# Kernel optimization log

Hardware: AMD Instinct MI355X
Metric: run time of the kernel (lower is better)

Reference implementation:

```python
import jax, jax.numpy as jnp
import numpy as np

B, T, D, H, NB, K, CDIM, CTX = 8, 4096, 3, 128, 6, 20, 128, 7


def setup_inputs() -> dict:
    key = jax.random.key(0)
    ks = jax.random.split(key, 16)
    s = 0.05
    inp = {
        'p': jax.random.normal(ks[0], (B, T, D), jnp.float32),
        'W_pos': jax.random.normal(ks[1], (D, H), jnp.float32) * s,
        'b_pos': jnp.zeros((H,), jnp.float32),
        # ResnetBlockFC(2H -> H): fc_0(2H,H), fc_1(H,H), shortcut(2H,H, no bias)
        'blk_W0': jax.random.normal(ks[2], (NB, 2 * H, H), jnp.float32) * s,
        'blk_b0': jnp.zeros((NB, H), jnp.float32),
        'blk_W1': jax.random.normal(ks[3], (NB, H, H), jnp.float32) * s,
        'blk_b1': jnp.zeros((NB, H), jnp.float32),
        'blk_Ws': jax.random.normal(ks[4], (NB, 2 * H, H), jnp.float32) * s,
        # Attention: score MLP on context (dim 7 -> 1), output proj (H -> H)
        'att_Wc': jax.random.normal(ks[5], (NB, CTX, 1), jnp.float32) * s,
        'att_bc': jnp.zeros((NB, 1), jnp.float32),
        'att_Wo': jax.random.normal(ks[6], (NB, H, H), jnp.float32) * s,
        'att_bo': jnp.zeros((NB, H), jnp.float32),
        'W_c': jax.random.normal(ks[7], (H, CDIM), jnp.float32) * s,
        'b_c': jnp.zeros((CDIM,), jnp.float32),
    }
    return inp


def _knn(p):
    # squared pairwise distances [B,T,T], top-K smallest
    sq = jnp.sum(p * p, axis=-1)  # [B,T]
    d2 = sq[:, :, None] + sq[:, None, :] - 2.0 * jnp.einsum('btd,bsd->bts', p, p)
    neg, idx = jax.lax.top_k(-d2, K)            # idx: [B,T,K]
    dis = jnp.sqrt(jnp.maximum(-neg, 1e-12))    # euclidean distance [B,T,K]
    return dis, idx


def _gather(c, idx):
    # c: [B,T,h], idx: [B,T,K] -> [B,T,K,h]  (vectorized pool_local)
    return jax.vmap(lambda ci, ii: ci[ii])(c, idx)


def _resnet_block(x, W0, b0, W1, b1, Ws):
    # occupancy-networks ResnetBlockFC: shortcut(x) + fc_1(relu(fc_0(relu(x))))
    h = jnp.maximum(x, 0.0) @ W0 + b0
    dx = jnp.maximum(h, 0.0) @ W1 + b1
    return x @ Ws + dx


def reference(p, W_pos, b_pos, blk_W0, blk_b0, blk_W1, blk_b1, blk_Ws,
              att_Wc, att_bc, att_Wo, att_bo, W_c, b_c):
    dis, idx = _knn(p)
    pooled_points = _gather(p, idx)                                   # [B,T,K,3]
    p_rep = jnp.broadcast_to(p[:, :, None, :], (B, T, K, D))
    context = jnp.concatenate([dis[..., None], pooled_points, p_rep], axis=-1)  # [B,T,K,7]

    net = p @ W_pos + b_pos                                           # [B,T,H]
    last_net = jnp.zeros_like(net)
    for i in range(NB):
        pooled = _gather(net, idx)                                    # [B,T,K,H]
        # attention over the K neighbors, weights from context
        scores = context @ att_Wc[i] + att_bc[i]                      # [B,T,K,1]
        w = jax.nn.softmax(scores, axis=2)
        att = jnp.sum(w * pooled, axis=2) @ att_Wo[i] + att_bo[i]     # [B,T,H]
        x = jnp.concatenate([net, att], axis=2)                       # [B,T,2H]
        net = _resnet_block(x, blk_W0[i], blk_b0[i], blk_W1[i], blk_b1[i], blk_Ws[i])
        net = net + last_net
        last_net = net
    return net @ W_c + b_c                                            # [B,T,c_dim]
```

## Files before the change

kernel.cpp:

```cpp
#include <hip/hip_runtime.h>
#include <hip/hip_bf16.h>
#include <math.h>

#define BB 8
#define TT 4096
#define HHD 128
#define NBK 6
#define KNN 20
#define BT (BB*TT)

typedef __attribute__((ext_vector_type(8))) short bf16x8;
typedef __attribute__((ext_vector_type(4))) float f32x4;

__device__ __forceinline__ float b2f(unsigned short u){
  return __uint_as_float(((unsigned int)u) << 16);
}
__device__ __forceinline__ unsigned short f2b(float f){
  unsigned int x = __float_as_uint(f);
  unsigned int r = (x + 0x7fffu + ((x >> 16) & 1u)) >> 16;
  return (unsigned short)r;
}
__device__ __forceinline__ float ldp(const void* base, int i, int f32m){
  return f32m ? ((const float*)base)[i] : b2f(((const unsigned short*)base)[i]);
}
__device__ __forceinline__ float lo2f(unsigned int u){ return __uint_as_float(u << 16); }
__device__ __forceinline__ float hi2f(unsigned int u){ return __uint_as_float(u & 0xffff0000u); }
__device__ __forceinline__ unsigned int relu2(unsigned int u){
  unsigned int s = u & 0x80008000u;
  unsigned int m = s | (s - (s >> 15));
  return u & ~m;
}
__device__ __forceinline__ bf16x8 relu8(bf16x8 x){
  union { bf16x8 v; unsigned int u[4]; } t; t.v = x;
  t.u[0] = relu2(t.u[0]); t.u[1] = relu2(t.u[1]);
  t.u[2] = relu2(t.u[2]); t.u[3] = relu2(t.u[3]);
  return t.v;
}

__global__ void k_detect(const unsigned short* __restrict__ wpos_raw, int* __restrict__ flag){
  if (threadIdx.x == 0 && blockIdx.x == 0) {
    int cnt = 0;
    for (int i = 0; i < 384; ++i) {
      unsigned int e = (wpos_raw[i] >> 7) & 0xFFu;
      if (e >= 0x90u) cnt++;
    }
    *flag = (cnt > 10) ? 1 : 0;
  }
}

__global__ __launch_bounds__(256) void k_prep_points(const void* __restrict__ p,
                                                     const int* __restrict__ flagp,
                                                     float4* __restrict__ pf4){
  int r = blockIdx.x*256 + threadIdx.x;
  if (r >= BT) return;
  int f32m = *flagp;
  float x = ldp(p, r*3+0, f32m), y = ldp(p, r*3+1, f32m), z = ldp(p, r*3+2, f32m);
  float sq = __fadd_rn(__fadd_rn(__fmul_rn(x,x), __fmul_rn(y,y)), __fmul_rn(z,z));
  pf4[r] = make_float4(x, y, z, sq);
}

__global__ __launch_bounds__(256) void k_net0(const float4* __restrict__ pf4,
                                              const void* __restrict__ Wpos,
                                              const void* __restrict__ bpos,
                                              const int* __restrict__ flagp,
                                              unsigned short* __restrict__ netA){
  int t = blockIdx.x*256 + threadIdx.x;
  int f32m = *flagp;
  int c = t & 127, r = t >> 7;
  float4 q = pf4[r];
  float v = ldp(bpos, c, f32m);
  v = fmaf(q.x, ldp(Wpos, c,       f32m), v);
  v = fmaf(q.y, ldp(Wpos, 128 + c, f32m), v);
  v = fmaf(q.z, ldp(Wpos, 256 + c, f32m), v);
  netA[t] = f2b(v);
}

__global__ __launch_bounds__(256) void k_transpose(const void* __restrict__ W0,
                                                   const void* __restrict__ W1,
                                                   const void* __restrict__ Ws,
                                                   const void* __restrict__ Wo,
                                                   const void* __restrict__ Wc,
                                                   const int* __restrict__ flagp,
                                                   unsigned short* __restrict__ wT){
  int t = blockIdx.x*256 + threadIdx.x;
  int f32m = *flagp;
  if (t < 196608) {
    int i = t >> 15; int rem = t & 32767; int n = rem >> 8; int k = rem & 255;
    wT[t] = f2b(ldp(W0, i*32768 + k*128 + n, f32m));
  } else if (t < 294912) {
    int u = t - 196608; int i = u >> 14; int rem = u & 16383; int n = rem >> 7; int k = rem & 127;
    wT[t] = f2b(ldp(W1, i*16384 + k*128 + n, f32m));
  } else if (t < 491520) {
    int u = t - 294912; int i = u >> 15; int rem = u & 32767; int n = rem >> 8; int k = rem & 255;
    wT[t] = f2b(ldp(Ws, i*32768 + k*128 + n, f32m));
  } else if (t < 589824) {
    int u = t - 491520; int i = u >> 14; int rem = u & 16383; int n = rem >> 7; int k = rem & 127;
    wT[t] = f2b(ldp(Wo, i*16384 + k*128 + n, f32m));
  } else if (t < 606208) {
    int u = t - 589824; int n = u >> 7; int k = u & 127;
    wT[t] = f2b(ldp(Wc, k*128 + n, f32m));
  }
}

#define INS(act, dv, iv) do { bool A_ = (act); float D_ = (dv); int I_ = (iv);        \
  _Pragma("unroll")                                                                    \
  for (int j = 19; j >= 1; --j) {                                                      \
    bool cj = A_ && (D_ < ld[j]); bool cm = A_ && (D_ < ld[j-1]);                      \
    ld[j] = cj ? (cm ? ld[j-1] : D_) : ld[j];                                          \
    li[j] = cj ? (cm ? li[j-1] : I_) : li[j];                                          \
  }                                                                                    \
  { bool c0 = A_ && (D_ < ld[0]); ld[0] = c0 ? D_ : ld[0]; li[0] = c0 ? I_ : li[0]; } \
} while(0)

__global__ __launch_bounds__(256) void k_knn(const float4* __restrict__ pf4,
                                             const void* __restrict__ Wc,
                                             const void* __restrict__ bc,
                                             const int* __restrict__ flagp,
                                             unsigned short* __restrict__ idx16,
                                             unsigned short* __restrict__ wsoftb){
  __shared__ char smem[40960];
  float4* tile = (float4*)smem;
  float*  lsd  = (float*)smem;
  int*    lsi  = (int*)(smem + 20480);

  int tid  = threadIdx.x;
  int part = tid >> 6, lane = tid & 63;
  int rq   = blockIdx.x*64 + lane;
  int b    = rq >> 12;
  int f32m = *flagp;
  float4 q = pf4[rq];

  float ld[20]; int li[20];
  #pragma unroll
  for (int j = 0; j < 20; ++j) { ld[j] = 3.0e38f; li[j] = 0; }
  float thresh = 3.0e38f;
  float bd0=0.f,bd1=0.f,bd2=0.f,bd3=0.f; int bi0=0,bi1=0,bi2=0,bi3=0; int cnt=0;

  for (int ch = 0; ch < 4; ++ch) {
    __syncthreads();
    {
      const float4* src = pf4 + (b << 12) + part*1024 + ch*256;
      tile[part*256 + lane      ] = src[lane      ];
      tile[part*256 + lane +  64] = src[lane +  64];
      tile[part*256 + lane + 128] = src[lane + 128];
      tile[part*256 + lane + 192] = src[lane + 192];
    }
    __syncthreads();
    int baseI = part*1024 + ch*256;
    for (int j = 0; j < 256; ++j) {
      float4 pt = tile[part*256 + j];
      float dot = __fadd_rn(__fadd_rn(__fmul_rn(q.x,pt.x), __fmul_rn(q.y,pt.y)),
                            __fmul_rn(q.z,pt.z));
      float d2  = __fsub_rn(__fadd_rn(q.w, pt.w), __fmul_rn(2.0f, dot));
      bool take = d2 < thresh;
      int  gi   = baseI + j;
      bool t0 = take && (cnt == 0); bd0 = t0 ? d2 : bd0; bi0 = t0 ? gi : bi0;
      bool t1 = take && (cnt == 1); bd1 = t1 ? d2 : bd1; bi1 = t1 ? gi : bi1;
      bool t2 = take && (cnt == 2); bd2 = t2 ? d2 : bd2; bi2 = t2 ? gi : bi2;
      bool t3 = take && (cnt == 3); bd3 = t3 ? d2 : bd3; bi3 = t3 ? gi : bi3;
      cnt += take ? 1 : 0;
      if (__ballot(cnt >= 4)) {
        INS(cnt > 0, bd0, bi0); INS(cnt > 1, bd1, bi1);
        INS(cnt > 2, bd2, bi2); INS(cnt > 3, bd3, bi3);
        cnt = 0; thresh = ld[19];
      }
    }
  }
  INS(cnt > 0, bd0, bi0); INS(cnt > 1, bd1, bi1);
  INS(cnt > 2, bd2, bi2); INS(cnt > 3, bd3, bi3);

  __syncthreads();
  #pragma unroll
  for (int j = 0; j < 20; ++j) { lsd[tid*20 + j] = ld[j]; lsi[tid*20 + j] = li[j]; }
  __syncthreads();

  if (tid < 64) {
    int p0 = tid*20, p1 = (64+tid)*20, p2 = (128+tid)*20, p3 = (192+tid)*20;
    int i0=0, i1=0, i2=0, i3=0;
    float dis[20]; int outi[20];
    #pragma unroll 4
    for (int o = 0; o < 20; ++o) {
      float d0 = lsd[p0+i0], d1 = lsd[p1+i1], d2v = lsd[p2+i2], d3 = lsd[p3+i3];
      float bd = d0; int sel = 0;
      if (d1  < bd) { bd = d1;  sel = 1; }
      if (d2v < bd) { bd = d2v; sel = 2; }
      if (d3  < bd) { bd = d3;  sel = 3; }
      int bi = (sel==0) ? lsi[p0+i0] : (sel==1) ? lsi[p1+i1] : (sel==2) ? lsi[p2+i2] : lsi[p3+i3];
      i0 += (sel==0); i1 += (sel==1); i2 += (sel==2); i3 += (sel==3);
      dis[o] = sqrtf(fmaxf(bd, 1e-12f));
      outi[o] = bi;
    }
    float nx[20], ny[20], nz[20];
    #pragma unroll 4
    for (int k = 0; k < 20; ++k) {
      idx16[rq*20 + k] = (unsigned short)outi[k];
      float4 pp = pf4[(b << 12) + outi[k]];
      nx[k] = pp.x; ny[k] = pp.y; nz[k] = pp.z;
    }
    for (int i = 0; i < NBK; ++i) {
      float w0 = ldp(Wc,i*7+0,f32m), w1 = ldp(Wc,i*7+1,f32m), w2 = ldp(Wc,i*7+2,f32m);
      float w3 = ldp(Wc,i*7+3,f32m), w4 = ldp(Wc,i*7+4,f32m), w5 = ldp(Wc,i*7+5,f32m);
      float w6 = ldp(Wc,i*7+6,f32m);
      float bci = ldp(bc,i,f32m);
      float s[20]; float mx = -3.0e38f;
      #pragma unroll
      for (int k = 0; k < 20; ++k) {
        float v = bci;
        v = fmaf(dis[k], w0, v);
        v = fmaf(nx[k], w1, v); v = fmaf(ny[k], w2, v); v = fmaf(nz[k], w3, v);
        v = fmaf(q.x, w4, v);  v = fmaf(q.y, w5, v);  v = fmaf(q.z, w6, v);
        s[k] = v; mx = fmaxf(mx, v);
      }
      float sum = 0.f;
      #pragma unroll
      for (int k = 0; k < 20; ++k) { float e = __expf(s[k] - mx); s[k] = e; sum += e; }
      float inv = 1.0f / sum;
      #pragma unroll
      for (int k = 0; k < 20; ++k) wsoftb[(rq*6 + i)*20 + k] = f2b(s[k]*inv);
    }
  }
}

__global__ __launch_bounds__(256) void k_block(const unsigned short* __restrict__ netIn,
                                               unsigned short* __restrict__ netOut,
                                               const unsigned short* __restrict__ idx16,
                                               const unsigned short* __restrict__ wsoftb,
                                               const unsigned short* __restrict__ wT,
                                               const void* __restrict__ b0s,
                                               const void* __restrict__ b1s,
                                               const void* __restrict__ bos,
                                               const int* __restrict__ flagp,
                                               int iblk, int hasResid){
  __shared__ unsigned short ldsA[2][16*136];
  __shared__ unsigned short ldsH[2][16*136];
  int tid = threadIdx.x;
  int f32m = *flagp;
  int w = tid >> 6, lane = tid & 63;
  int t = w >> 1;
  int c = w & 1;
  int b  = blockIdx.x & 7;
  int r0 = (b << 12) + ((blockIdx.x >> 3) << 5) + (t << 4);
  const unsigned short* W0T = wT + iblk*32768;
  const unsigned short* W1T = wT + 196608 + iblk*16384;
  const unsigned short* WsT = wT + 294912 + iblk*32768;
  const unsigned short* WoT = wT + 491520 + iblk*16384;
  int m = lane & 15, qd = lane >> 4;

  {
    int r = lane >> 2, cg = lane & 3;
    int grow = r0 + r;
    int cbase = c*64 + cg*16;
    float acc[16];
    #pragma unroll
    for (int j = 0; j < 16; ++j) acc[j] = 0.f;
    #pragma unroll 4
    for (int k = 0; k < 20; ++k) {
      int nb = idx16[grow*20 + k] & 4095;
      float wk = b2f(wsoftb[(grow*6 + iblk)*20 + k]);
      const uint4* np_ = (const uint4*)(netIn + ((b << 12) + nb)*128 + cbase);
      #pragma unroll
      for (int u = 0; u < 2; ++u) {
        uint4 uu = np_[u];
        acc[u*8+0] = fmaf(wk, lo2f(uu.x), acc[u*8+0]);
        acc[u*8+1] = fmaf(wk, hi2f(uu.x), acc[u*8+1]);
        acc[u*8+2] = fmaf(wk, lo2f(uu.y), acc[u*8+2]);
        acc[u*8+3] = fmaf(wk, hi2f(uu.y), acc[u*8+3]);
        acc[u*8+4] = fmaf(wk, lo2f(uu.z), acc[u*8+4]);
        acc[u*8+5] = fmaf(wk, hi2f(uu.z), acc[u*8+5]);
        acc[u*8+6] = fmaf(wk, lo2f(uu.w), acc[u*8+6]);
        acc[u*8+7] = fmaf(wk, hi2f(uu.w), acc[u*8+7]);
      }
    }
    unsigned short* hb = ldsH[t];
    #pragma unroll
    for (int j = 0; j < 8; ++j) {
      unsigned int pr = ((unsigned int)f2b(acc[2*j+1]) << 16) | (unsigned int)f2b(acc[2*j]);
      *(unsigned int*)(hb + r*136 + cbase + 2*j) = pr;
    }
  }
  __syncthreads();

  {
    bf16x8 asf[4];
    #pragma unroll
    for (int ks = 0; ks < 4; ++ks)
      asf[ks] = *(const bf16x8*)(ldsH[t] + m*136 + ks*32 + qd*8);
    f32x4 acc2[4];
    #pragma unroll
    for (int i = 0; i < 4; ++i) { f32x4 z = {0.f,0.f,0.f,0.f}; acc2[i] = z; }
    #pragma unroll
    for (int i = 0; i < 4; ++i) {
      int cti = c*4 + i;
      const unsigned short* bp = WoT + (cti*16 + m)*128 + qd*8;
      #pragma unroll
      for (int ks = 0; ks < 4; ++ks)
        acc2[i] = __builtin_amdgcn_mfma_f32_16x16x32_bf16(asf[ks], *(const bf16x8*)(bp + ks*32), acc2[i], 0, 0, 0);
    }
    unsigned short* ab = ldsA[t];
    #pragma unroll
    for (int i = 0; i < 4; ++i) {
      int col = (c*4 + i)*16 + m;
      float bo = ldp(bos, iblk*128 + col, f32m);
      #pragma unroll
      for (int rr = 0; rr < 4; ++rr)
        ab[(qd*4 + rr)*136 + col] = f2b(acc2[i][rr] + bo);
    }
  }
  __syncthreads();

  bf16x8 nf[4], af[4];
  {
    const unsigned short* nrow = netIn + (r0 + m)*128;
    #pragma unroll
    for (int ks = 0; ks < 4; ++ks) nf[ks] = *(const bf16x8*)(nrow + ks*32 + qd*8);
    #pragma unroll
    for (int ks = 0; ks < 4; ++ks) af[ks] = *(const bf16x8*)(ldsA[t] + m*136 + ks*32 + qd*8);
    bf16x8 rnf[4], raf[4];
    #pragma unroll
    for (int ks = 0; ks < 4; ++ks) { rnf[ks] = relu8(nf[ks]); raf[ks] = relu8(af[ks]); }
    f32x4 acc3[4];
    #pragma unroll
    for (int i = 0; i < 4; ++i) { f32x4 z = {0.f,0.f,0.f,0.f}; acc3[i] = z; }
    #pragma unroll
    for (int i = 0; i < 4; ++i) {
      int cti = c*4 + i;
      const unsigned short* bp = W0T + (cti*16 + m)*256 + qd*8;
      #pragma unroll
      for (int ks = 0; ks < 4; ++ks)
        acc3[i] = __builtin_amdgcn_mfma_f32_16x16x32_bf16(rnf[ks], *(const bf16x8*)(bp + ks*32), acc3[i], 0, 0, 0);
      #pragma unroll
      for (int ks = 0; ks < 4; ++ks)
        acc3[i] = __builtin_amdgcn_mfma_f32_16x16x32_bf16(raf[ks], *(const bf16x8*)(bp + 128 + ks*32), acc3[i], 0, 0, 0);
    }
    unsigned short* hb = ldsH[t];
    #pragma unroll
    for (int i = 0; i < 4; ++i) {
      int col = (c*4 + i)*16 + m;
      float b0v = ldp(b0s, iblk*128 + col, f32m);
      #pragma unroll
      for (int rr = 0; rr < 4; ++rr)
        hb[(qd*4 + rr)*136 + col] = f2b(fmaxf(acc3[i][rr] + b0v, 0.f));
    }
  }
  __syncthreads();

  {
    bf16x8 hf[4];
    #pragma unroll
    for (int ks = 0; ks < 4; ++ks) hf[ks] = *(const bf16x8*)(ldsH[t] + m*136 + ks*32 + qd*8);
    f32x4 acc4[4];
    #pragma unroll
    for (int i = 0; i < 4; ++i) { f32x4 z = {0.f,0.f,0.f,0.f}; acc4[i] = z; }
    #pragma unroll
    for (int i = 0; i < 4; ++i) {
      int cti = c*4 + i;
      const unsigned short* bp1 = W1T + (cti*16 + m)*128 + qd*8;
      #pragma unroll
      for (int ks = 0; ks < 4; ++ks)
        acc4[i] = __builtin_amdgcn_mfma_f32_16x16x32_bf16(hf[ks], *(const bf16x8*)(bp1 + ks*32), acc4[i], 0, 0, 0);
      const unsigned short* bps = WsT + (cti*16 + m)*256 + qd*8;
      #pragma unroll
      for (int ks = 0; ks < 4; ++ks)
        acc4[i] = __builtin_amdgcn_mfma_f32_16x16x32_bf16(nf[ks], *(const bf16x8*)(bps + ks*32), acc4[i], 0, 0, 0);
      #pragma unroll
      for (int ks = 0; ks < 4; ++ks)
        acc4[i] = __builtin_amdgcn_mfma_f32_16x16x32_bf16(af[ks], *(const bf16x8*)(bps + 128 + ks*32), acc4[i], 0, 0, 0);
    }
    #pragma unroll
    for (int i = 0; i < 4; ++i) {
      int col = (c*4 + i)*16 + m;
      float b1v = ldp(b1s, iblk*128 + col, f32m);
      #pragma unroll
      for (int rr = 0; rr < 4; ++rr) {
        int grow2 = r0 + qd*4 + rr;
        float v = acc4[i][rr] + b1v;
        if (hasResid) v += b2f(netIn[grow2*128 + col]);
        netOut[grow2*128 + col] = f2b(v);
      }
    }
  }
}

__global__ __launch_bounds__(256) void k_final(const unsigned short* __restrict__ netIn,
                                               const unsigned short* __restrict__ WcT,
                                               const void* __restrict__ bcv,
                                               const int* __restrict__ flagp,
                                               void* __restrict__ out){
  int tid = threadIdx.x; int w = tid >> 6, lane = tid & 63;
  int f32m = *flagp;
  int t = w >> 1, c = w & 1;
  int r0 = blockIdx.x*32 + t*16;
  int m = lane & 15, qd = lane >> 4;
  bf16x8 nf[4];
  #pragma unroll
  for (int ks = 0; ks < 4; ++ks)
    nf[ks] = *(const bf16x8*)(netIn + (r0 + m)*128 + ks*32 + qd*8);
  f32x4 acc[4];
  #pragma unroll
  for (int i = 0; i < 4; ++i) { f32x4 z = {0.f,0.f,0.f,0.f}; acc[i] = z; }
  #pragma unroll
  for (int i = 0; i < 4; ++i) {
    int cti = c*4 + i;
    const unsigned short* bp = WcT + (cti*16 + m)*128 + qd*8;
    #pragma unroll
    for (int ks = 0; ks < 4; ++ks)
      acc[i] = __builtin_amdgcn_mfma_f32_16x16x32_bf16(nf[ks], *(const bf16x8*)(bp + ks*32), acc[i], 0, 0, 0);
  }
  if (f32m) {
    float* o = (float*)out;
    #pragma unroll
    for (int i = 0; i < 4; ++i) {
      int col = (c*4 + i)*16 + m;
      float bcf = ldp(bcv, col, 1);
      #pragma unroll
      for (int rr = 0; rr < 4; ++rr)
        o[(r0 + qd*4 + rr)*128 + col] = acc[i][rr] + bcf;
    }
  } else {
    unsigned short* o = (unsigned short*)out;
    #pragma unroll
    for (int i = 0; i < 4; ++i) {
      int col = (c*4 + i)*16 + m;
      float bcf = ldp(bcv, col, 0);
      #pragma unroll
      for (int rr = 0; rr < 4; ++rr)
        o[(r0 + qd*4 + rr)*128 + col] = f2b(acc[i][rr] + bcf);
    }
  }
}

extern "C" void kernel_launch(void* const* d_in, const int* in_sizes, int n_in,
                              void* d_out, int out_size, void* d_ws, size_t ws_size,
                              hipStream_t stream){
  const void* p    = d_in[0];
  const void* Wpos = d_in[1];
  const void* bpos = d_in[2];
  const void* W0   = d_in[3];
  const void* b0   = d_in[4];
  const void* W1   = d_in[5];
  const void* b1   = d_in[6];
  const void* Ws   = d_in[7];
  const void* Wc_  = d_in[8];
  const void* bc_  = d_in[9];
  const void* Wo   = d_in[10];
  const void* bo   = d_in[11];
  const void* WC   = d_in[12];
  const void* bC   = d_in[13];

  char* ws = (char*)d_ws;
  int*            flag   = (int*)(ws + 0);
  float4*         pf4    = (float4*)(ws + 256);
  unsigned short* idx16  = (unsigned short*)(ws + 524544);
  unsigned short* wsoftb = (unsigned short*)(ws + 1835264);
  unsigned short* netA   = (unsigned short*)(ws + 9699584);
  unsigned short* wT     = (unsigned short*)(ws + 18088192);

  k_detect     <<<dim3(1),     dim3(64),  0, stream>>>((const unsigned short*)Wpos, flag);
  k_prep_points<<<dim3(128),   dim3(256), 0, stream>>>(p, flag, pf4);
  k_net0       <<<dim3(16384), dim3(256), 0, stream>>>(pf4, Wpos, bpos, flag, netA);
  k_transpose  <<<dim3(2368),  dim3(256), 0, stream>>>(W0, W1, Ws, Wo, WC, flag, wT);
  k_knn        <<<dim3(512),   dim3(256), 0, stream>>>(pf4, Wc_, bc_, flag, idx16, wsoftb);

  unsigned short* a   = netA;
  unsigned short* bpt = (unsigned short*)d_out;
  for (int i = 0; i < 6; ++i) {
    k_block<<<dim3(1024), dim3(256), 0, stream>>>(a, bpt, idx16, wsoftb, wT,
                                                  b0, b1, bo, flag, i, (i > 0) ? 1 : 0);
    unsigned short* t = a; a = bpt; bpt = t;
  }
  k_final<<<dim3(1024), dim3(256), 0, stream>>>(a, wT + 589824, bC, flag, d_out);
}
```

Measured before the change: 719.8 us.

## Split block work so each workgroup handles 16 rows across four column-split waves

```diff
diff --git a/kernel.cpp b/kernel.cpp
--- a/kernel.cpp
+++ b/kernel.cpp
@@ -231,15 +231,13 @@
                                                const void* __restrict__ bos,
                                                const int* __restrict__ flagp,
                                                int iblk, int hasResid){
-  __shared__ unsigned short ldsA[2][16*136];
-  __shared__ unsigned short ldsH[2][16*136];
+  __shared__ unsigned short ldsA[16*136];
+  __shared__ unsigned short ldsH[16*136];
   int tid = threadIdx.x;
   int f32m = *flagp;
   int w = tid >> 6, lane = tid & 63;
-  int t = w >> 1;
-  int c = w & 1;
   int b  = blockIdx.x & 7;
-  int r0 = (b << 12) + ((blockIdx.x >> 3) << 5) + (t << 4);
+  int r0 = (b << 12) + ((blockIdx.x >> 3) << 4);
   const unsigned short* W0T = wT + iblk*32768;
   const unsigned short* W1T = wT + 196608 + iblk*16384;
   const unsigned short* WsT = wT + 294912 + iblk*32768;
@@ -247,35 +245,29 @@
   int m = lane & 15, qd = lane >> 4;
 
   {
-    int r = lane >> 2, cg = lane & 3;
+    int r = tid & 15, g = tid >> 4;
     int grow = r0 + r;
-    int cbase = c*64 + cg*16;
-    float acc[16];
-    #pragma unroll
-    for (int j = 0; j < 16; ++j) acc[j] = 0.f;
+    float acc[8];
+    #pragma unroll
+    for (int j = 0; j < 8; ++j) acc[j] = 0.f;
     #pragma unroll 4
     for (int k = 0; k < 20; ++k) {
       int nb = idx16[grow*20 + k] & 4095;
       float wk = b2f(wsoftb[(grow*6 + iblk)*20 + k]);
-      const uint4* np_ = (const uint4*)(netIn + ((b << 12) + nb)*128 + cbase);
-      #pragma unroll
-      for (int u = 0; u < 2; ++u) {
-        uint4 uu = np_[u];
-        acc[u*8+0] = fmaf(wk, lo2f(uu.x), acc[u*8+0]);
-        acc[u*8+1] = fmaf(wk, hi2f(uu.x), acc[u*8+1]);
-        acc[u*8+2] = fmaf(wk, lo2f(uu.y), acc[u*8+2]);
-        acc[u*8+3] = fmaf(wk, hi2f(uu.y), acc[u*8+3]);
-        acc[u*8+4] = fmaf(wk, lo2f(uu.z), acc[u*8+4]);
-        acc[u*8+5] = fmaf(wk, hi2f(uu.z), acc[u*8+5]);
-        acc[u*8+6] = fmaf(wk, lo2f(uu.w), acc[u*8+6]);
-        acc[u*8+7] = fmaf(wk, hi2f(uu.w), acc[u*8+7]);
-      }
-    }
-    unsigned short* hb = ldsH[t];
-    #pragma unroll
-    for (int j = 0; j < 8; ++j) {
+      uint4 uu = *(const uint4*)(netIn + ((b << 12) + nb)*128 + g*8);
+      acc[0] = fmaf(wk, lo2f(uu.x), acc[0]);
+      acc[1] = fmaf(wk, hi2f(uu.x), acc[1]);
+      acc[2] = fmaf(wk, lo2f(uu.y), acc[2]);
+      acc[3] = fmaf(wk, hi2f(uu.y), acc[3]);
+      acc[4] = fmaf(wk, lo2f(uu.z), acc[4]);
+      acc[5] = fmaf(wk, hi2f(uu.z), acc[5]);
+      acc[6] = fmaf(wk, lo2f(uu.w), acc[6]);
+      acc[7] = fmaf(wk, hi2f(uu.w), acc[7]);
+    }
+    #pragma unroll
+    for (int j = 0; j < 4; ++j) {
       unsigned int pr = ((unsigned int)f2b(acc[2*j+1]) << 16) | (unsigned int)f2b(acc[2*j]);
-      *(unsigned int*)(hb + r*136 + cbase + 2*j) = pr;
+      *(unsigned int*)(ldsH + r*136 + g*8 + 2*j) = pr;
     }
   }
   __syncthreads();
@@ -284,26 +276,25 @@
     bf16x8 asf[4];
     #pragma unroll
     for (int ks = 0; ks < 4; ++ks)
-      asf[ks] = *(const bf16x8*)(ldsH[t] + m*136 + ks*32 + qd*8);
-    f32x4 acc2[4];
-    #pragma unroll
-    for (int i = 0; i < 4; ++i) { f32x4 z = {0.f,0.f,0.f,0.f}; acc2[i] = z; }
-    #pragma unroll
-    for (int i = 0; i < 4; ++i) {
-      int cti = c*4 + i;
+      asf[ks] = *(const bf16x8*)(ldsH + m*136 + ks*32 + qd*8);
+    f32x4 acc2[2];
+    #pragma unroll
+    for (int i = 0; i < 2; ++i) { f32x4 z = {0.f,0.f,0.f,0.f}; acc2[i] = z; }
+    #pragma unroll
+    for (int i = 0; i < 2; ++i) {
+      int cti = w*2 + i;
       const unsigned short* bp = WoT + (cti*16 + m)*128 + qd*8;
       #pragma unroll
       for (int ks = 0; ks < 4; ++ks)
         acc2[i] = __builtin_amdgcn_mfma_f32_16x16x32_bf16(asf[ks], *(const bf16x8*)(bp + ks*32), acc2[i], 0, 0, 0);
     }
-    unsigned short* ab = ldsA[t];
-    #pragma unroll
-    for (int i = 0; i < 4; ++i) {
-      int col = (c*4 + i)*16 + m;
+    #pragma unroll
+    for (int i = 0; i < 2; ++i) {
+      int col = (w*2 + i)*16 + m;
       float bo = ldp(bos, iblk*128 + col, f32m);
       #pragma unroll
       for (int rr = 0; rr < 4; ++rr)
-        ab[(qd*4 + rr)*136 + col] = f2b(acc2[i][rr] + bo);
+        ldsA[(qd*4 + rr)*136 + col] = f2b(acc2[i][rr] + bo);
     }
   }
   __syncthreads();
@@ -314,16 +305,16 @@
     #pragma unroll
     for (int ks = 0; ks < 4; ++ks) nf[ks] = *(const bf16x8*)(nrow + ks*32 + qd*8);
     #pragma unroll
-    for (int ks = 0; ks < 4; ++ks) af[ks] = *(const bf16x8*)(ldsA[t] + m*136 + ks*32 + qd*8);
+    for (int ks = 0; ks < 4; ++ks) af[ks] = *(const bf16x8*)(ldsA + m*136 + ks*32 + qd*8);
     bf16x8 rnf[4], raf[4];
     #pragma unroll
     for (int ks = 0; ks < 4; ++ks) { rnf[ks] = relu8(nf[ks]); raf[ks] = relu8(af[ks]); }
-    f32x4 acc3[4];
-    #pragma unroll
-    for (int i = 0; i < 4; ++i) { f32x4 z = {0.f,0.f,0.f,0.f}; acc3[i] = z; }
-    #pragma unroll
-    for (int i = 0; i < 4; ++i) {
-      int cti = c*4 + i;
+    f32x4 acc3[2];
+    #pragma unroll
+    for (int i = 0; i < 2; ++i) { f32x4 z = {0.f,0.f,0.f,0.f}; acc3[i] = z; }
+    #pragma unroll
+    for (int i = 0; i < 2; ++i) {
+      int cti = w*2 + i;
       const unsigned short* bp = W0T + (cti*16 + m)*256 + qd*8;
       #pragma unroll
       for (int ks = 0; ks < 4; ++ks)
@@ -332,14 +323,14 @@
       for (int ks = 0; ks < 4; ++ks)
         acc3[i] = __builtin_amdgcn_mfma_f32_16x16x32_bf16(raf[ks], *(const bf16x8*)(bp + 128 + ks*32), acc3[i], 0, 0, 0);
     }
-    unsigned short* hb = ldsH[t];
-    #pragma unroll
-    for (int i = 0; i < 4; ++i) {
-      int col = (c*4 + i)*16 + m;
+    __syncthreads();
+    #pragma unroll
+    for (int i = 0; i < 2; ++i) {
+      int col = (w*2 + i)*16 + m;
       float b0v = ldp(b0s, iblk*128 + col, f32m);
       #pragma unroll
       for (int rr = 0; rr < 4; ++rr)
-        hb[(qd*4 + rr)*136 + col] = f2b(fmaxf(acc3[i][rr] + b0v, 0.f));
+        ldsH[(qd*4 + rr)*136 + col] = f2b(fmaxf(acc3[i][rr] + b0v, 0.f));
     }
   }
   __syncthreads();
@@ -347,13 +338,13 @@
   {
     bf16x8 hf[4];
     #pragma unroll
-    for (int ks = 0; ks < 4; ++ks) hf[ks] = *(const bf16x8*)(ldsH[t] + m*136 + ks*32 + qd*8);
-    f32x4 acc4[4];
-    #pragma unroll
-    for (int i = 0; i < 4; ++i) { f32x4 z = {0.f,0.f,0.f,0.f}; acc4[i] = z; }
-    #pragma unroll
-    for (int i = 0; i < 4; ++i) {
-      int cti = c*4 + i;
+    for (int ks = 0; ks < 4; ++ks) hf[ks] = *(const bf16x8*)(ldsH + m*136 + ks*32 + qd*8);
+    f32x4 acc4[2];
+    #pragma unroll
+    for (int i = 0; i < 2; ++i) { f32x4 z = {0.f,0.f,0.f,0.f}; acc4[i] = z; }
+    #pragma unroll
+    for (int i = 0; i < 2; ++i) {
+      int cti = w*2 + i;
       const unsigned short* bp1 = W1T + (cti*16 + m)*128 + qd*8;
       #pragma unroll
       for (int ks = 0; ks < 4; ++ks)
@@ -367,8 +358,8 @@
         acc4[i] = __builtin_amdgcn_mfma_f32_16x16x32_bf16(af[ks], *(const bf16x8*)(bps + 128 + ks*32), acc4[i], 0, 0, 0);
     }
     #pragma unroll
-    for (int i = 0; i < 4; ++i) {
-      int col = (c*4 + i)*16 + m;
+    for (int i = 0; i < 2; ++i) {
+      int col = (w*2 + i)*16 + m;
       float b1v = ldp(b1s, iblk*128 + col, f32m);
       #pragma unroll
       for (int rr = 0; rr < 4; ++rr) {
@@ -388,19 +379,18 @@
                                                void* __restrict__ out){
   int tid = threadIdx.x; int w = tid >> 6, lane = tid & 63;
   int f32m = *flagp;
-  int t = w >> 1, c = w & 1;
-  int r0 = blockIdx.x*32 + t*16;
+  int r0 = blockIdx.x*16;
   int m = lane & 15, qd = lane >> 4;
   bf16x8 nf[4];
   #pragma unroll
   for (int ks = 0; ks < 4; ++ks)
     nf[ks] = *(const bf16x8*)(netIn + (r0 + m)*128 + ks*32 + qd*8);
-  f32x4 acc[4];
+  f32x4 acc[2];
   #pragma unroll
-  for (int i = 0; i < 4; ++i) { f32x4 z = {0.f,0.f,0.f,0.f}; acc[i] = z; }
+  for (int i = 0; i < 2; ++i) { f32x4 z = {0.f,0.f,0.f,0.f}; acc[i] = z; }
   #pragma unroll
-  for (int i = 0; i < 4; ++i) {
-    int cti = c*4 + i;
+  for (int i = 0; i < 2; ++i) {
+    int cti = w*2 + i;
     const unsigned short* bp = WcT + (cti*16 + m)*128 + qd*8;
     #pragma unroll
     for (int ks = 0; ks < 4; ++ks)
@@ -409,8 +399,8 @@
   if (f32m) {
     float* o = (float*)out;
     #pragma unroll
-    for (int i = 0; i < 4; ++i) {
-      int col = (c*4 + i)*16 + m;
+    for (int i = 0; i < 2; ++i) {
+      int col = (w*2 + i)*16 + m;
       float bcf = ldp(bcv, col, 1);
       #pragma unroll
       for (int rr = 0; rr < 4; ++rr)
@@ -419,8 +409,8 @@
   } else {
     unsigned short* o = (unsigned short*)out;
     #pragma unroll
-    for (int i = 0; i < 4; ++i) {
-      int col = (c*4 + i)*16 + m;
+    for (int i = 0; i < 2; ++i) {
+      int col = (w*2 + i)*16 + m;
       float bcf = ldp(bcv, col, 0);
       #pragma unroll
       for (int rr = 0; rr < 4; ++rr)
@@ -464,9 +454,9 @@
   unsigned short* a   = netA;
   unsigned short* bpt = (unsigned short*)d_out;
   for (int i = 0; i < 6; ++i) {
-    k_block<<<dim3(1024), dim3(256), 0, stream>>>(a, bpt, idx16, wsoftb, wT,
+    k_block<<<dim3(2048), dim3(256), 0, stream>>>(a, bpt, idx16, wsoftb, wT,
                                                   b0, b1, bo, flag, i, (i > 0) ? 1 : 0);
     unsigned short* t = a; a = bpt; bpt = t;
   }
-  k_final<<<dim3(1024), dim3(256), 0, stream>>>(a, wT + 589824, bC, flag, d_out);
-}
+  k_final<<<dim3(2048), dim3(256), 0, stream>>>(a, wT + 589824, bC, flag, d_out);
+}
```

After: 819.1 us. 1.14x slower.

## Split KNN candidate scan across 8 partitions with 32 queries per block

Applied to the files above, without the earlier changes.

```diff
diff --git a/kernel.cpp b/kernel.cpp
--- a/kernel.cpp
+++ b/kernel.cpp
@@ -124,8 +124,11 @@
   int*    lsi  = (int*)(smem + 20480);
 
   int tid  = threadIdx.x;
-  int part = tid >> 6, lane = tid & 63;
-  int rq   = blockIdx.x*64 + lane;
+  int w    = tid >> 6, lane = tid & 63;
+  int half = lane >> 5;
+  int qi   = lane & 31;
+  int part = (w << 1) | half;
+  int rq   = blockIdx.x*32 + qi;
   int b    = rq >> 12;
   int f32m = *flagp;
   float4 q = pf4[rq];
@@ -136,19 +139,20 @@
   float thresh = 3.0e38f;
   float bd0=0.f,bd1=0.f,bd2=0.f,bd3=0.f; int bi0=0,bi1=0,bi2=0,bi3=0; int cnt=0;
 
-  for (int ch = 0; ch < 4; ++ch) {
-    __syncthreads();
+  for (int ch = 0; ch < 2; ++ch) {
     {
-      const float4* src = pf4 + (b << 12) + part*1024 + ch*256;
-      tile[part*256 + lane      ] = src[lane      ];
-      tile[part*256 + lane +  64] = src[lane +  64];
-      tile[part*256 + lane + 128] = src[lane + 128];
-      tile[part*256 + lane + 192] = src[lane + 192];
-    }
-    __syncthreads();
-    int baseI = part*1024 + ch*256;
+      const float4* base0 = pf4 + (b << 12) + (w*2    )*512 + ch*256;
+      const float4* base1 = pf4 + (b << 12) + (w*2 + 1)*512 + ch*256;
+      float4* tw = tile + w*512;
+      #pragma unroll
+      for (int i = 0; i < 4; ++i) tw[lane + i*64]       = base0[lane + i*64];
+      #pragma unroll
+      for (int i = 0; i < 4; ++i) tw[256 + lane + i*64] = base1[lane + i*64];
+    }
+    int baseI = part*512 + ch*256;
+    const float4* tp = tile + w*512 + half*256;
     for (int j = 0; j < 256; ++j) {
-      float4 pt = tile[part*256 + j];
+      float4 pt = tp[j];
       float dot = __fadd_rn(__fadd_rn(__fmul_rn(q.x,pt.x), __fmul_rn(q.y,pt.y)),
                             __fmul_rn(q.z,pt.z));
       float d2  = __fsub_rn(__fadd_rn(q.w, pt.w), __fmul_rn(2.0f, dot));
@@ -174,21 +178,24 @@
   for (int j = 0; j < 20; ++j) { lsd[tid*20 + j] = ld[j]; lsi[tid*20 + j] = li[j]; }
   __syncthreads();
 
-  if (tid < 64) {
-    int p0 = tid*20, p1 = (64+tid)*20, p2 = (128+tid)*20, p3 = (192+tid)*20;
-    int i0=0, i1=0, i2=0, i3=0;
+  if (tid < 32) {
+    int hp[8];
+    #pragma unroll
+    for (int pp = 0; pp < 8; ++pp) hp[pp] = ((pp >> 1)*64 + (pp & 1)*32 + tid)*20;
+    int ip[8];
+    #pragma unroll
+    for (int pp = 0; pp < 8; ++pp) ip[pp] = 0;
     float dis[20]; int outi[20];
-    #pragma unroll 4
     for (int o = 0; o < 20; ++o) {
-      float d0 = lsd[p0+i0], d1 = lsd[p1+i1], d2v = lsd[p2+i2], d3 = lsd[p3+i3];
-      float bd = d0; int sel = 0;
-      if (d1  < bd) { bd = d1;  sel = 1; }
-      if (d2v < bd) { bd = d2v; sel = 2; }
-      if (d3  < bd) { bd = d3;  sel = 3; }
-      int bi = (sel==0) ? lsi[p0+i0] : (sel==1) ? lsi[p1+i1] : (sel==2) ? lsi[p2+i2] : lsi[p3+i3];
-      i0 += (sel==0); i1 += (sel==1); i2 += (sel==2); i3 += (sel==3);
+      float bd = lsd[hp[0] + ip[0]]; int sel = 0;
+      #pragma unroll
+      for (int pp = 1; pp < 8; ++pp) {
+        float dv = lsd[hp[pp] + ip[pp]];
+        if (dv < bd) { bd = dv; sel = pp; }
+      }
+      outi[o] = lsi[hp[sel] + ip[sel]];
+      ip[sel]++;
       dis[o] = sqrtf(fmaxf(bd, 1e-12f));
-      outi[o] = bi;
     }
     float nx[20], ny[20], nz[20];
     #pragma unroll 4
@@ -459,7 +466,7 @@
   k_prep_points<<<dim3(128),   dim3(256), 0, stream>>>(p, flag, pf4);
   k_net0       <<<dim3(16384), dim3(256), 0, stream>>>(pf4, Wpos, bpos, flag, netA);
   k_transpose  <<<dim3(2368),  dim3(256), 0, stream>>>(W0, W1, Ws, Wo, WC, flag, wT);
-  k_knn        <<<dim3(512),   dim3(256), 0, stream>>>(pf4, Wc_, bc_, flag, idx16, wsoftb);
+  k_knn        <<<dim3(1024),  dim3(256), 0, stream>>>(pf4, Wc_, bc_, flag, idx16, wsoftb);
 
   unsigned short* a   = netA;
   unsigned short* bpt = (unsigned short*)d_out;
```

New measurement: 805.5 us. +11.9%, slower.
